# Optimization experiments

Measured on AMD Instinct MI355X. Metric: run time of the kernel, lower is better.

The kernel has to match this reference:

```python
import jax, jax.numpy as jnp
import numpy as np

B, C, H, W = 4, 256, 128, 128
OUT = 50

def setup_inputs() -> dict:
    key = jax.random.key(0)
    k1, k2, k3 = jax.random.split(key, 3)
    x = jax.random.normal(k1, (B, C, H, W), dtype=jnp.float32)
    # conv2d 1x1 weights, kaiming-ish scale
    W_f = jax.random.normal(k2, (OUT, C), dtype=jnp.float32) * (1.0 / np.sqrt(C))
    W_beta = jax.random.normal(k3, (C, C), dtype=jnp.float32) * (1.0 / np.sqrt(C))
    return {"x": x, "W_f": W_f, "W_beta": W_beta}

def reference(x, W_f, W_beta):
    b, c, h, w = x.shape
    n = h * w
    xf = x.reshape(b, c, n)                      # [B,C,N]
    F = jnp.einsum('oc,bcn->bon', W_f, xf)       # 1x1 conv -> [B,O,N]
    # S = softmax(F @ A, axis over C), A = xf^T : [B,N,C]
    S = jnp.einsum('bon,bcn->boc', F, xf)        # [B,O,C]
    S = jax.nn.softmax(S, axis=2)
    St = jnp.swapaxes(S, 1, 2)                   # [B,C,O]
    E = jnp.einsum('bco,bon->bcn', St, F)        # [B,C,N]
    E = E.reshape(b, c, h, w)
    E = jnp.einsum('dc,bchw->bdhw', W_beta, E) + x  # beta conv + residual
    return E
```

## Files before the change

### kernel.cpp

```cpp
#include <hip/hip_runtime.h>
#include <math.h>

#define CCH 256
#define OCH 50
#define NPIX 16384
#define BATCH 4
#define BO (BATCH*OCH)
#define NSPLIT2 128
#define KC2 (NPIX/NSPLIT2)

typedef _Float16 f16x8 __attribute__((ext_vector_type(8)));
typedef float f32x4 __attribute__((ext_vector_type(4)));
typedef unsigned int uint;
typedef unsigned short ushort;

__device__ __forceinline__ void cvt_split(const float4 v0, const float4 v1,
                                          f16x8& h, f16x8& l) {
    float v[8] = {v0.x, v0.y, v0.z, v0.w, v1.x, v1.y, v1.z, v1.w};
#pragma unroll
    for (int j = 0; j < 8; ++j) {
        _Float16 hj = (_Float16)v[j];
        h[j] = hj;
        l[j] = (_Float16)(v[j] - (float)hj);
    }
}

__device__ __forceinline__ uint packhl(float v) {
    _Float16 h = (_Float16)v;
    _Float16 l = (_Float16)(v - (float)h);
    union { _Float16 f; ushort u; } H, L;
    H.f = h; L.f = l;
    return (uint)H.u | ((uint)L.u << 16);
}

__device__ __forceinline__ void unpack8(const uint* w, f16x8& h, f16x8& l) {
    union { uint u[4]; f16x8 v; } H, L;
#pragma unroll
    for (int k = 0; k < 4; ++k) {
        H.u[k] = __builtin_amdgcn_perm(w[2 * k + 1], w[2 * k], 0x05040100u);
        L.u[k] = __builtin_amdgcn_perm(w[2 * k + 1], w[2 * k], 0x07060302u);
    }
    h = H.v; l = L.v;
}

__global__ void k0_pack(const float* __restrict__ Wf, uint* __restrict__ Wf16p) {
    int i = blockIdx.x * 256 + threadIdx.x;
    if (i < 64 * CCH) {
        int o = i / CCH;
        float v = (o < OCH) ? Wf[i] : 0.f;
        Wf16p[i] = packhl(v);
    }
}

__global__ __launch_bounds__(256) void k1_mfma(const float* __restrict__ x,
                                               const uint* __restrict__ Wf16p,
                                               float* __restrict__ F) {
    int b  = blockIdx.y;
    int p0 = blockIdx.x * 64;
    int t  = threadIdx.x;
    int w = t >> 6, lane = t & 63, r16 = lane & 15, kg = lane >> 4;
    __shared__ uint xl[2][32 * 64];

    int cidx = t & 15;
    int pixg = t >> 4;
    const float* xb = x + ((size_t)b * CCH) * NPIX + p0;

    float4 r0 = *(const float4*)(xb + (size_t)cidx * NPIX + pixg * 4);
    float4 r1 = *(const float4*)(xb + (size_t)(16 + cidx) * NPIX + pixg * 4);

    f32x4 acc[4];
#pragma unroll
    for (int nt = 0; nt < 4; ++nt) acc[nt] = {0.f, 0.f, 0.f, 0.f};

    const uint* Arow = Wf16p + (w * 16 + r16) * CCH;

#pragma unroll
    for (int s = 0; s < 8; ++s) {
        uint* buf = xl[s & 1];
        float v0[4] = {r0.x, r0.y, r0.z, r0.w};
        float v1[4] = {r1.x, r1.y, r1.z, r1.w};
#pragma unroll
        for (int j = 0; j < 4; ++j) {
            int pix = pixg * 4 + j;
            int q = (pix & 7) << 2;
            buf[pix * 32 + (cidx ^ q)]        = packhl(v0[j]);
            buf[pix * 32 + ((16 + cidx) ^ q)] = packhl(v1[j]);
        }
        if (s < 7) {
            r0 = *(const float4*)(xb + (size_t)((s + 1) * 32 + cidx) * NPIX + pixg * 4);
            r1 = *(const float4*)(xb + (size_t)((s + 1) * 32 + 16 + cidx) * NPIX + pixg * 4);
        }
        __syncthreads();

        uint aw[8];
        *(uint4*)aw       = *(const uint4*)(Arow + s * 32 + kg * 8);
        *(uint4*)(aw + 4) = *(const uint4*)(Arow + s * 32 + kg * 8 + 4);
        f16x8 Ah, Al;
        unpack8(aw, Ah, Al);

#pragma unroll
        for (int nt = 0; nt < 4; ++nt) {
            int pix = nt * 16 + r16;
            int q = (r16 & 7) << 2;
            uint bw[8];
            *(uint4*)bw       = *(const uint4*)&buf[pix * 32 + ((kg * 8) ^ q)];
            *(uint4*)(bw + 4) = *(const uint4*)&buf[pix * 32 + ((kg * 8 + 4) ^ q)];
            f16x8 Bh, Bl;
            unpack8(bw, Bh, Bl);
            acc[nt] = __builtin_amdgcn_mfma_f32_16x16x32_f16(Ah, Bh, acc[nt], 0, 0, 0);
            acc[nt] = __builtin_amdgcn_mfma_f32_16x16x32_f16(Ah, Bl, acc[nt], 0, 0, 0);
            acc[nt] = __builtin_amdgcn_mfma_f32_16x16x32_f16(Al, Bh, acc[nt], 0, 0, 0);
        }
    }

    float* Fb = F + ((size_t)b * 64 + w * 16 + kg * 4) * NPIX + p0;
#pragma unroll
    for (int nt = 0; nt < 4; ++nt)
#pragma unroll
        for (int r = 0; r < 4; ++r)
            Fb[(size_t)r * NPIX + nt * 16 + r16] = acc[nt][r];
}

__global__ __launch_bounds__(256) void k2_mfma(const float* __restrict__ x,
                                               const float* __restrict__ F,
                                               float* __restrict__ Spart) {
    int ks = blockIdx.x;
    int b  = blockIdx.y;
    int ch = blockIdx.z;
    int wave = threadIdx.x >> 6;
    int lane = threadIdx.x & 63;
    int r16  = lane & 15;
    int kg   = lane >> 4;
    int n0   = ks * KC2;

    f32x4 acc[8];
#pragma unroll
    for (int nt = 0; nt < 8; ++nt) acc[nt] = {0.f, 0.f, 0.f, 0.f};

    const float* Ab = F + ((size_t)b * 64 + wave * 16 + r16) * NPIX + n0 + kg * 8;
    const float* Bb = x + ((size_t)b * CCH + ch * 128 + r16) * NPIX + n0 + kg * 8;

#pragma unroll
    for (int kk = 0; kk < KC2 / 32; ++kk) {
        const float* ap = Ab + kk * 32;
        f16x8 ah, al;
        cvt_split(*(const float4*)ap, *(const float4*)(ap + 4), ah, al);
#pragma unroll
        for (int nt = 0; nt < 8; ++nt) {
            const float* bp = Bb + (size_t)nt * 16 * NPIX + kk * 32;
            f16x8 bh, bl;
            cvt_split(*(const float4*)bp, *(const float4*)(bp + 4), bh, bl);
            acc[nt] = __builtin_amdgcn_mfma_f32_16x16x32_f16(ah, bh, acc[nt], 0, 0, 0);
            acc[nt] = __builtin_amdgcn_mfma_f32_16x16x32_f16(ah, bl, acc[nt], 0, 0, 0);
            acc[nt] = __builtin_amdgcn_mfma_f32_16x16x32_f16(al, bh, acc[nt], 0, 0, 0);
        }
    }
    float* Sp = Spart + (((size_t)ks * BATCH + b) * 64 + wave * 16 + kg * 4) * 256
              + ch * 128 + r16;
#pragma unroll
    for (int nt = 0; nt < 8; ++nt)
#pragma unroll
        for (int r = 0; r < 4; ++r)
            Sp[(size_t)r * 256 + nt * 16] = acc[nt][r];
}

__global__ __launch_bounds__(1024) void k2r_softmax(const float* __restrict__ Spart,
                                                    float* __restrict__ S) {
    int row = blockIdx.x;
    int b = row / OCH, o = row % OCH;
    int tid = threadIdx.x;
    int c = tid & 255, g = tid >> 8;
    __shared__ float part[4][CCH];
    __shared__ float red[8];
    float v = 0.f;
    const size_t ksStride = (size_t)BATCH * 64 * 256;
    const float* p = Spart + ((size_t)(g * (NSPLIT2 / 4)) * BATCH + b) * 64 * 256
                   + (size_t)o * 256 + c;
#pragma unroll 8
    for (int ks = 0; ks < NSPLIT2 / 4; ++ks)
        v += p[ks * ksStride];
    part[g][c] = v;
    __syncthreads();
    float vv = 0.f, e = 0.f, m;
    if (tid < 256) {
        vv = part[0][c] + part[1][c] + part[2][c] + part[3][c];
        m = vv;
#pragma unroll
        for (int off = 32; off > 0; off >>= 1) m = fmaxf(m, __shfl_xor(m, off, 64));
        if ((tid & 63) == 0) red[tid >> 6] = m;
    }
    __syncthreads();
    if (tid < 256) {
        m = fmaxf(fmaxf(red[0], red[1]), fmaxf(red[2], red[3]));
        e = expf(vv - m);
        float s = e;
#pragma unroll
        for (int off = 32; off > 0; off >>= 1) s += __shfl_xor(s, off, 64);
        if ((tid & 63) == 0) red[4 + (tid >> 6)] = s;
    }
    __syncthreads();
    if (tid < 256) {
        float tot = red[4] + red[5] + red[6] + red[7];
        S[(size_t)row * CCH + c] = e / tot;
    }
}

__global__ __launch_bounds__(256) void k3_M(const float* __restrict__ Wbeta,
                                            const float* __restrict__ S,
                                            float* __restrict__ Mt) {
    int row = blockIdx.x;
    int d = threadIdx.x;
    const float* srow = S + (size_t)row * CCH;
    const float4* wb = (const float4*)(Wbeta + (size_t)d * CCH);
    float acc = 0.f;
#pragma unroll 4
    for (int cg = 0; cg < CCH / 4; ++cg) {
        float4 w = wb[cg];
        float4 s = *(const float4*)(srow + cg * 4);
        acc += w.x * s.x + w.y * s.y + w.z * s.z + w.w * s.w;
    }
    Mt[(size_t)row * CCH + d] = acc;
}

__global__ __launch_bounds__(256) void k4_out(const float* __restrict__ x,
                                              const float* __restrict__ F,
                                              const float* __restrict__ Mt,
                                              float* __restrict__ out) {
    int b  = blockIdx.z;
    int dq = blockIdx.y;
    int n  = blockIdx.x * 256 + threadIdx.x;
    float acc[32];
#pragma unroll
    for (int dd = 0; dd < 32; ++dd) acc[dd] = 0.f;
    const float* Fp = F + (size_t)b * 64 * NPIX + n;
    const float* mt = Mt + (size_t)b * OCH * CCH + dq * 32;
#pragma unroll 2
    for (int o = 0; o < OCH; ++o) {
        float fo = Fp[(size_t)o * NPIX];
        const float* m = mt + o * CCH;
#pragma unroll
        for (int dd = 0; dd < 32; ++dd) acc[dd] = fmaf(m[dd], fo, acc[dd]);
    }
    const float* xp = x + ((size_t)b * CCH + dq * 32) * NPIX + n;
    float* op = out + ((size_t)b * CCH + dq * 32) * NPIX + n;
#pragma unroll
    for (int dd = 0; dd < 32; ++dd)
        __builtin_nontemporal_store(acc[dd] + xp[(size_t)dd * NPIX], &op[(size_t)dd * NPIX]);
}

extern "C" void kernel_launch(void* const* d_in, const int* in_sizes, int n_in,
                              void* d_out, int out_size, void* d_ws, size_t ws_size,
                              hipStream_t stream) {
    const float* x     = (const float*)d_in[0];
    const float* Wf    = (const float*)d_in[1];
    const float* Wbeta = (const float*)d_in[2];
    float* out = (float*)d_out;

    float* F     = (float*)d_ws;
    uint*  Wf16p = (uint*)(F + (size_t)BATCH * 64 * NPIX);
    float* S     = (float*)(Wf16p + 64 * CCH);
    float* Mt    = S + (size_t)BO * CCH;
    float* Spart = out;

    k0_pack<<<dim3((64 * CCH + 255) / 256), dim3(256), 0, stream>>>(Wf, Wf16p);
    k1_mfma<<<dim3(NPIX / 64, BATCH), dim3(256), 0, stream>>>(x, Wf16p, F);
    k2_mfma<<<dim3(NSPLIT2, BATCH, 2), dim3(256), 0, stream>>>(x, F, Spart);
    k2r_softmax<<<dim3(BO), dim3(1024), 0, stream>>>(Spart, S);
    k3_M<<<dim3(BO), dim3(256), 0, stream>>>(Wbeta, S, Mt);
    k4_out<<<dim3(NPIX / 256, 8, BATCH), dim3(256), 0, stream>>>(x, F, Mt, out);
}
```

Baseline: 202.8 us.

## Software-pipeline k1 LDS staging and k2 global loads; double k2 split count

```diff
diff --git a/kernel.cpp b/kernel.cpp
--- a/kernel.cpp
+++ b/kernel.cpp
@@ -6,7 +6,7 @@
 #define NPIX 16384
 #define BATCH 4
 #define BO (BATCH*OCH)
-#define NSPLIT2 128
+#define NSPLIT2 256
 #define KC2 (NPIX/NSPLIT2)
 
 typedef _Float16 f16x8 __attribute__((ext_vector_type(8)));
@@ -74,30 +74,32 @@
 
     const uint* Arow = Wf16p + (w * 16 + r16) * CCH;
 
-#pragma unroll
-    for (int s = 0; s < 8; ++s) {
-        uint* buf = xl[s & 1];
+    {
         float v0[4] = {r0.x, r0.y, r0.z, r0.w};
         float v1[4] = {r1.x, r1.y, r1.z, r1.w};
 #pragma unroll
         for (int j = 0; j < 4; ++j) {
             int pix = pixg * 4 + j;
             int q = (pix & 7) << 2;
-            buf[pix * 32 + (cidx ^ q)]        = packhl(v0[j]);
-            buf[pix * 32 + ((16 + cidx) ^ q)] = packhl(v1[j]);
-        }
+            xl[0][pix * 32 + (cidx ^ q)]        = packhl(v0[j]);
+            xl[0][pix * 32 + ((16 + cidx) ^ q)] = packhl(v1[j]);
+        }
+    }
+    __syncthreads();
+
+#pragma unroll
+    for (int s = 0; s < 8; ++s) {
         if (s < 7) {
             r0 = *(const float4*)(xb + (size_t)((s + 1) * 32 + cidx) * NPIX + pixg * 4);
             r1 = *(const float4*)(xb + (size_t)((s + 1) * 32 + 16 + cidx) * NPIX + pixg * 4);
         }
-        __syncthreads();
-
         uint aw[8];
         *(uint4*)aw       = *(const uint4*)(Arow + s * 32 + kg * 8);
         *(uint4*)(aw + 4) = *(const uint4*)(Arow + s * 32 + kg * 8 + 4);
         f16x8 Ah, Al;
         unpack8(aw, Ah, Al);
 
+        const uint* buf = xl[s & 1];
 #pragma unroll
         for (int nt = 0; nt < 4; ++nt) {
             int pix = nt * 16 + r16;
@@ -111,6 +113,19 @@
             acc[nt] = __builtin_amdgcn_mfma_f32_16x16x32_f16(Ah, Bl, acc[nt], 0, 0, 0);
             acc[nt] = __builtin_amdgcn_mfma_f32_16x16x32_f16(Al, Bh, acc[nt], 0, 0, 0);
         }
+        if (s < 7) {
+            float v0[4] = {r0.x, r0.y, r0.z, r0.w};
+            float v1[4] = {r1.x, r1.y, r1.z, r1.w};
+            uint* nbuf = xl[(s + 1) & 1];
+#pragma unroll
+            for (int j = 0; j < 4; ++j) {
+                int pix = pixg * 4 + j;
+                int q = (pix & 7) << 2;
+                nbuf[pix * 32 + (cidx ^ q)]        = packhl(v0[j]);
+                nbuf[pix * 32 + ((16 + cidx) ^ q)] = packhl(v1[j]);
+            }
+            __syncthreads();
+        }
     }
 
     float* Fb = F + ((size_t)b * 64 + w * 16 + kg * 4) * NPIX + p0;
@@ -133,27 +148,41 @@
     int kg   = lane >> 4;
     int n0   = ks * KC2;
 
+    const float* Ab = F + ((size_t)b * 64 + wave * 16 + r16) * NPIX + n0 + kg * 8;
+    f16x8 Ah0, Al0, Ah1, Al1;
+    cvt_split(*(const float4*)Ab, *(const float4*)(Ab + 4), Ah0, Al0);
+    cvt_split(*(const float4*)(Ab + 32), *(const float4*)(Ab + 36), Ah1, Al1);
+
+    const float* Bb = x + ((size_t)b * CCH + ch * 128 + r16) * NPIX + n0 + kg * 8;
+    float4 c0 = *(const float4*)(Bb);
+    float4 c1 = *(const float4*)(Bb + 4);
+    float4 c2 = *(const float4*)(Bb + 32);
+    float4 c3 = *(const float4*)(Bb + 36);
+
     f32x4 acc[8];
 #pragma unroll
     for (int nt = 0; nt < 8; ++nt) acc[nt] = {0.f, 0.f, 0.f, 0.f};
 
-    const float* Ab = F + ((size_t)b * 64 + wave * 16 + r16) * NPIX + n0 + kg * 8;
-    const float* Bb = x + ((size_t)b * CCH + ch * 128 + r16) * NPIX + n0 + kg * 8;
-
-#pragma unroll
-    for (int kk = 0; kk < KC2 / 32; ++kk) {
-        const float* ap = Ab + kk * 32;
-        f16x8 ah, al;
-        cvt_split(*(const float4*)ap, *(const float4*)(ap + 4), ah, al);
-#pragma unroll
-        for (int nt = 0; nt < 8; ++nt) {
-            const float* bp = Bb + (size_t)nt * 16 * NPIX + kk * 32;
-            f16x8 bh, bl;
-            cvt_split(*(const float4*)bp, *(const float4*)(bp + 4), bh, bl);
-            acc[nt] = __builtin_amdgcn_mfma_f32_16x16x32_f16(ah, bh, acc[nt], 0, 0, 0);
-            acc[nt] = __builtin_amdgcn_mfma_f32_16x16x32_f16(ah, bl, acc[nt], 0, 0, 0);
-            acc[nt] = __builtin_amdgcn_mfma_f32_16x16x32_f16(al, bh, acc[nt], 0, 0, 0);
-        }
+#pragma unroll
+    for (int nt = 0; nt < 8; ++nt) {
+        float4 p0_, p1_, p2_, p3_;
+        if (nt < 7) {
+            const float* bp = Bb + (size_t)(nt + 1) * 16 * NPIX;
+            p0_ = *(const float4*)(bp);
+            p1_ = *(const float4*)(bp + 4);
+            p2_ = *(const float4*)(bp + 32);
+            p3_ = *(const float4*)(bp + 36);
+        }
+        f16x8 bh, bl;
+        cvt_split(c0, c1, bh, bl);
+        acc[nt] = __builtin_amdgcn_mfma_f32_16x16x32_f16(Ah0, bh, acc[nt], 0, 0, 0);
+        acc[nt] = __builtin_amdgcn_mfma_f32_16x16x32_f16(Ah0, bl, acc[nt], 0, 0, 0);
+        acc[nt] = __builtin_amdgcn_mfma_f32_16x16x32_f16(Al0, bh, acc[nt], 0, 0, 0);
+        cvt_split(c2, c3, bh, bl);
+        acc[nt] = __builtin_amdgcn_mfma_f32_16x16x32_f16(Ah1, bh, acc[nt], 0, 0, 0);
+        acc[nt] = __builtin_amdgcn_mfma_f32_16x16x32_f16(Ah1, bl, acc[nt], 0, 0, 0);
+        acc[nt] = __builtin_amdgcn_mfma_f32_16x16x32_f16(Al1, bh, acc[nt], 0, 0, 0);
+        if (nt < 7) { c0 = p0_; c1 = p1_; c2 = p2_; c3 = p3_; }
     }
     float* Sp = Spart + (((size_t)ks * BATCH + b) * 64 + wave * 16 + kg * 4) * 256
               + ch * 128 + r16;
```

Result: no change. 202.2 us (-0.3%).
